# Performance work log

Measured on AMD Instinct MI355X. Metric: run time of the kernel, lower is better.

## Reference

```python
import jax, jax.numpy as jnp
import numpy as np

B, S, D, H, DK, F, L, FEAT, T = 32, 256, 512, 8, 64, 2048, 6, 9, 100


def _pos_emb(seq_len, d):
    # 'transformers from scratch' style sinusoidal embedding
    pos = jnp.arange(seq_len, dtype=jnp.float32)[:, None]
    dim = jnp.arange(d, dtype=jnp.float32)[None, :]
    phase = pos / jnp.power(1e4, dim / d)
    return jnp.where(jnp.arange(d)[None, :] % 2 == 0, jnp.sin(phase), jnp.cos(phase))


def _ln(x, g, b, eps=1e-5):
    m = jnp.mean(x, -1, keepdims=True)
    v = jnp.mean((x - m) ** 2, -1, keepdims=True)
    return (x - m) * jax.lax.rsqrt(v + eps) * g + b


def _mha(q_in, k_in, v_in, wq, bq, wk, bk, wv, bv, wo, bo):
    # wq/wk/wv: [H, D, DK]; batched equivalent of per-head Linear projections
    q = jnp.einsum('bsd,hdk->bhsk', q_in, wq) + bq[:, None, :]
    k = jnp.einsum('bsd,hdk->bhsk', k_in, wk) + bk[:, None, :]
    v = jnp.einsum('bsd,hdk->bhsk', v_in, wv) + bv[:, None, :]
    scale = jnp.sqrt(jnp.asarray(q.shape[-1], jnp.float32))
    att = jax.nn.softmax(jnp.einsum('bhqk,bhsk->bhqs', q, k) / scale, axis=-1)
    o = jnp.einsum('bhqs,bhsv->bhqv', att, v)  # [B,H,S,DK]
    o = o.transpose(0, 2, 1, 3).reshape(q_in.shape[0], q_in.shape[1], -1)  # concat heads
    return o @ wo + bo


def setup_inputs() -> dict:
    key = jax.random.key(0)
    ks = iter(jax.random.split(key, 64))
    rn = lambda *sh: 0.02 * jax.random.normal(next(ks), sh, jnp.float32)
    d = {
        'tgt': jax.random.uniform(next(ks), (B, S, FEAT), jnp.float32),
        'memory': jax.random.normal(next(ks), (B, S, D), jnp.float32),
        'time': jax.random.randint(next(ks), (B, S), 0, T),
        'gender': jax.random.randint(next(ks), (B, 1), 0, 2),
        'race': jax.random.randint(next(ks), (B, 1), 0, 3),
        'mask': jax.random.uniform(next(ks), (B, S, FEAT), jnp.float32),
        'w_f2h': rn(FEAT, D), 'b_f2h': jnp.zeros((D,)),
        'emb_time': rn(T, D), 'emb_gender': rn(2, D), 'emb_race': rn(3, D),
        'wq1': rn(L, H, D, DK), 'bq1': jnp.zeros((L, H, DK)),
        'wk1': rn(L, H, D, DK), 'bk1': jnp.zeros((L, H, DK)),
        'wv1': rn(L, H, D, DK), 'bv1': jnp.zeros((L, H, DK)),
        'wo1': rn(L, H * DK, D), 'bo1': jnp.zeros((L, D)),
        'g1': jnp.ones((L, D)), 'be1': jnp.zeros((L, D)),
        'wq2': rn(L, H, D, DK), 'bq2': jnp.zeros((L, H, DK)),
        'wk2': rn(L, H, D, DK), 'bk2': jnp.zeros((L, H, DK)),
        'wv2': rn(L, H, D, DK), 'bv2': jnp.zeros((L, H, DK)),
        'wo2': rn(L, H * DK, D), 'bo2': jnp.zeros((L, D)),
        'g2': jnp.ones((L, D)), 'be2': jnp.zeros((L, D)),
        'w1f': rn(L, D, F), 'b1f': jnp.zeros((L, F)),
        'w2f': rn(L, F, D), 'b2f': jnp.zeros((L, D)),
        'gf': jnp.ones((L, D)), 'bff': jnp.zeros((L, D)),
        'w_out': rn(D, FEAT), 'b_out': jnp.zeros((FEAT,)),
        'w_m': rn(D, FEAT), 'b_m': jnp.zeros((FEAT,)),
    }
    return d


def reference(tgt, memory, time, gender, race, mask,
              w_f2h, b_f2h, emb_time, emb_gender, emb_race,
              wq1, bq1, wk1, bk1, wv1, bv1, wo1, bo1, g1, be1,
              wq2, bq2, wk2, bk2, wv2, bv2, wo2, bo2, g2, be2,
              w1f, b1f, w2f, b2f, gf, bff,
              w_out, b_out, w_m, b_m):
    # attentioned_mask=False, mask provided -> tgt = tgt * mask
    x = (tgt * mask) @ w_f2h + b_f2h  # feature2hidden
    x = x + _pos_emb(x.shape[1], x.shape[2])
    x = x + emb_time[time] + emb_gender[gender] + emb_race[race]  # [B,S,D] += [B,1,D]
    for l in range(L):
        # self-attention residual block (dropout is identity in eval)
        x = _ln(x + _mha(x, x, x, wq1[l], bq1[l], wk1[l], bk1[l], wv1[l], bv1[l], wo1[l], bo1[l]), g1[l], be1[l])
        # 'cross' block: q,k from memory, v from tgt; residual on tgt (tensors[-1])
        x = _ln(x + _mha(memory, memory, x, wq2[l], bq2[l], wk2[l], bk2[l], wv2[l], bv2[l], wo2[l], bo2[l]), g2[l], be2[l])
        # feed forward
        x = _ln(x + jax.nn.relu(x @ w1f[l] + b1f[l]) @ w2f[l] + b2f[l], gf[l], bff[l])
    output = jax.nn.sigmoid(x @ w_out + b_out)
    mask_out = jax.nn.sigmoid(x @ w_m + b_m)  # attentioned_mask=False -> linear_m(tgt)
    return output, time, mask_out
```

## Files before the change

kernel.cpp:

```cpp
#include <hip/hip_runtime.h>
#include <hip/hip_bf16.h>
#include <math.h>

constexpr int Bn   = 32;
constexpr int Sn   = 256;
constexpr int Dn   = 512;
constexpr int Hn   = 8;
constexpr int DKn  = 64;
constexpr int Fn   = 2048;
constexpr int Ln   = 6;
constexpr int FEATn= 9;
constexpr int BSn  = Bn * Sn;

typedef __hip_bfloat16 bf16;
typedef __attribute__((ext_vector_type(8))) short short8;
typedef __attribute__((ext_vector_type(4))) short short4v;
typedef __attribute__((ext_vector_type(4))) float f32x4;

#define GLOAD_LDS16(gp, lp)                                                   \
    __builtin_amdgcn_global_load_lds(                                         \
        (const __attribute__((address_space(1))) void*)(gp),                  \
        (__attribute__((address_space(3))) void*)(lp), 16, 0, 0)

#define BARRIER do {                                                          \
    __builtin_amdgcn_sched_barrier(0);                                        \
    asm volatile("" ::: "memory");                                            \
    __builtin_amdgcn_s_barrier();                                             \
    asm volatile("" ::: "memory");                                            \
    __builtin_amdgcn_sched_barrier(0);                                        \
} while (0)

#define VMCNT0 do {                                                           \
    asm volatile("s_waitcnt vmcnt(0)" ::: "memory");                          \
    __builtin_amdgcn_sched_barrier(0);                                        \
} while (0)

#define LGKM0 do {                                                            \
    asm volatile("s_waitcnt lgkmcnt(0)" ::: "memory");                        \
    __builtin_amdgcn_sched_barrier(0);                                        \
} while (0)

__device__ __forceinline__ short f2bs(float f) {
    __hip_bfloat16 h = __float2bfloat16(f);
    return *reinterpret_cast<short*>(&h);
}
__device__ __forceinline__ float bs2f(short s) {
    unsigned u = ((unsigned)(unsigned short)s) << 16;
    return *reinterpret_cast<float*>(&u);
}

__global__ __launch_bounds__(256)
void k_embed(const float* __restrict__ tgt, const float* __restrict__ mask,
             const float* __restrict__ w_f2h, const float* __restrict__ b_f2h,
             const int* __restrict__ timei, const int* __restrict__ gender,
             const int* __restrict__ race,
             const float* __restrict__ emb_t, const float* __restrict__ emb_g,
             const float* __restrict__ emb_r, bf16* __restrict__ x)
{
    int idx = blockIdx.x * 256 + threadIdx.x;
    int d  = idx & (Dn - 1);
    int bs = idx >> 9;
    int b  = bs / Sn;
    int s  = bs & (Sn - 1);
    const float* tg = tgt  + (size_t)bs * FEATn;
    const float* mk = mask + (size_t)bs * FEATn;
    float acc = b_f2h[d];
    #pragma unroll
    for (int f = 0; f < FEATn; ++f) acc += tg[f] * mk[f] * w_f2h[f * Dn + d];
    float phase = (float)s * expf(-((float)d / (float)Dn) * 9.210340372f);
    acc += (d & 1) ? cosf(phase) : sinf(phase);
    acc += emb_t[(size_t)timei[bs] * Dn + d];
    acc += emb_g[(size_t)gender[b] * Dn + d];
    acc += emb_r[(size_t)race[b]   * Dn + d];
    x[idx] = __float2bfloat16(acc);
}

__global__ __launch_bounds__(256)
void k_cvt(const float* __restrict__ in, bf16* __restrict__ out)
{
    int i = blockIdx.x * 256 + threadIdx.x;
    out[i] = __float2bfloat16(in[i]);
}

__global__ __launch_bounds__(256)
void k_tcvt6(const float* __restrict__ i0, bf16* __restrict__ o0,
             const float* __restrict__ i1, bf16* __restrict__ o1,
             const float* __restrict__ i2, bf16* __restrict__ o2,
             const float* __restrict__ i3, bf16* __restrict__ o3,
             const float* __restrict__ i4, bf16* __restrict__ o4,
             const float* __restrict__ i5, bf16* __restrict__ o5,
             int R, int C, int ZB)
{
    __shared__ float ts[32][33];
    const int sel = blockIdx.z / ZB, zi = blockIdx.z % ZB;
    const float* in  = sel == 0 ? i0 : sel == 1 ? i1 : sel == 2 ? i2
                     : sel == 3 ? i3 : sel == 4 ? i4 : i5;
    bf16*        out = sel == 0 ? o0 : sel == 1 ? o1 : sel == 2 ? o2
                     : sel == 3 ? o3 : sel == 4 ? o4 : o5;
    const int t  = threadIdx.x;
    const int tx = t & 31, ty = t >> 5;
    const int r0 = blockIdx.y * 32, c0 = blockIdx.x * 32;
    const size_t zo = (size_t)zi * R * C;
    #pragma unroll
    for (int i = 0; i < 4; ++i)
        ts[ty + 8 * i][tx] = in[zo + (size_t)(r0 + ty + 8 * i) * C + c0 + tx];
    __syncthreads();
    #pragma unroll
    for (int i = 0; i < 4; ++i)
        out[zo + (size_t)(c0 + ty + 8 * i) * R + r0 + tx] =
            __float2bfloat16(ts[tx][ty + 8 * i]);
}

__global__ __launch_bounds__(256)
void k_prep_final(const float* __restrict__ w_out, const float* __restrict__ b_out,
                  const float* __restrict__ w_m, const float* __restrict__ b_m,
                  bf16* __restrict__ Wcat, float* __restrict__ bcat)
{
    int idx = blockIdx.x * 256 + threadIdx.x;
    int n = idx >> 9, k = idx & 511;
    float v = 0.f;
    if (n < FEATn)          v = w_out[(size_t)k * FEATn + n];
    else if (n < 2 * FEATn) v = w_m[(size_t)k * FEATn + (n - FEATn)];
    Wcat[idx] = __float2bfloat16(v);
    if (idx < 32) {
        float bv = idx < FEATn ? b_out[idx]
                 : (idx < 2 * FEATn ? b_m[idx - FEATn] : 0.f);
        bcat[idx] = bv;
    }
}

template<int BM, int BN, bool RELU, bool RESID, bool TRANSV = false>
__global__ __launch_bounds__(256)
void k_gemm_bf(const bf16* __restrict__ A0, const bf16* __restrict__ A1,
               const bf16* __restrict__ A2,
               const bf16* __restrict__ W0, const bf16* __restrict__ W1,
               const bf16* __restrict__ W2,
               const float* __restrict__ bi0, const float* __restrict__ bi1,
               const float* __restrict__ bi2,
               const bf16* __restrict__ R,
               bf16* __restrict__ C0, bf16* __restrict__ C1, bf16* __restrict__ C2,
               int M, int N, int K, int MTt, int NTt, int ZN, int stat)
{
    constexpr int WTM = BM / 2, WTN = BN / 2;
    constexpr int MT  = WTM / 16, NT = WTN / 16;
    constexpr int NCA = BM / 64;
    constexpr int NCB = BN / 64;
    constexpr int CSTR   = BN + 8;
    constexpr int PASSES = BM / 64;

    const int id = blockIdx.x;
    const int c  = id & 7, j = id >> 3;
    int mt, nt, z;
    if (stat == 0) {
        const int inner = NTt * ZN;
        const int ml = j / inner, r = j - ml * inner;
        mt = c * (MTt >> 3) + ml;
        nt = r % NTt;
        z  = r / NTt;
    } else {
        const int inner = MTt * ZN;
        const int nl = j / inner, r = j - nl * inner;
        nt = c * (NTt >> 3) + nl;
        mt = r % MTt;
        z  = r / MTt;
    }
    const int m0 = mt * BM, n0 = nt * BN;

    const short* A   = (const short*)(z == 0 ? A0 : (z == 1 ? A1 : A2));
    const short* W   = (const short*)(z == 0 ? W0 : (z == 1 ? W1 : W2));
    const float* bia = (z == 0 ? bi0 : (z == 1 ? bi1 : bi2));
    bf16*        C   = (z == 0 ? C0 : (z == 1 ? C1 : C2));

    __shared__ __align__(16) short As[BM * 32];
    __shared__ __align__(16) short Bs[BN * 32];
    __shared__ __align__(16) short Cs[64 * CSTR];

    const int t    = threadIdx.x;
    const int w    = t >> 6, lane = t & 63;
    const int l16  = lane & 15, quad = lane >> 4;
    const int wm   = (w & 1) * WTM, wn = (w >> 1) * WTN;

    const short* Agp[NCA];
    const short* Bgp[NCB];
    #pragma unroll
    for (int i = 0; i < NCA; ++i) {
        const int cc = w * BM + i * 64 + lane;
        Agp[i] = A + (size_t)(m0 + (cc >> 2)) * K + (cc & 3) * 8;
    }
    #pragma unroll
    for (int i = 0; i < NCB; ++i) {
        const int cc = w * BN + i * 64 + lane;
        Bgp[i] = W + (size_t)(n0 + (cc >> 2)) * K + (cc & 3) * 8;
    }

    f32x4 acc[MT][NT] = {};
    const bool tv = TRANSV && (z == 2);

    for (int k0 = 0; k0 < K; k0 += 32) {
        #pragma unroll
        for (int i = 0; i < NCA; ++i) {
            GLOAD_LDS16(Agp[i], As + (w * BM + i * 64) * 8);
            Agp[i] += 32;
        }
        #pragma unroll
        for (int i = 0; i < NCB; ++i) {
            GLOAD_LDS16(Bgp[i], Bs + (w * BN + i * 64) * 8);
            Bgp[i] += 32;
        }
        __syncthreads();

        short8 af[MT], bf[NT];
        #pragma unroll
        for (int mi = 0; mi < MT; ++mi)
            af[mi] = *(const short8*)(As + (wm + mi * 16 + l16) * 32 + quad * 8);
        #pragma unroll
        for (int ni = 0; ni < NT; ++ni)
            bf[ni] = *(const short8*)(Bs + (wn + ni * 16 + l16) * 32 + quad * 8);
        if (tv) {
            #pragma unroll
            for (int mi = 0; mi < MT; ++mi)
                #pragma unroll
                for (int ni = 0; ni < NT; ++ni)
                    acc[mi][ni] = __builtin_amdgcn_mfma_f32_16x16x32_bf16(
                        bf[ni], af[mi], acc[mi][ni], 0, 0, 0);
        } else {
            #pragma unroll
            for (int mi = 0; mi < MT; ++mi)
                #pragma unroll
                for (int ni = 0; ni < NT; ++ni)
                    acc[mi][ni] = __builtin_amdgcn_mfma_f32_16x16x32_bf16(
                        af[mi], bf[ni], acc[mi][ni], 0, 0, 0);
        }
        __syncthreads();
    }

    if (tv) {
        constexpr int CPR = BM / 8;
        #pragma unroll
        for (int p = 0; p < PASSES; ++p) {
            if (PASSES == 1 || wn == p * 64) {
                #pragma unroll
                for (int ni = 0; ni < NT; ++ni) {
                    #pragma unroll
                    for (int r = 0; r < 4; ++r) {
                        const int lrow = wn - p * 64 + ni * 16 + quad * 4 + r;
                        const float bb = bia[n0 + p * 64 + lrow];
                        #pragma unroll
                        for (int mi = 0; mi < MT; ++mi)
                            Cs[lrow * CSTR + wm + mi * 16 + l16] =
                                f2bs(acc[mi][ni][r] + bb);
                    }
                }
            }
            __syncthreads();
            #pragma unroll
            for (int cc = 0; cc < 64 * CPR; cc += 256) {
                const int row = (cc + t) / CPR, colc = (cc + t) % CPR;
                short8 cv = *(const short8*)(Cs + row * CSTR + colc * 8);
                *(short8*)((short*)C + (size_t)(n0 + p * 64 + row) * M
                                      + m0 + colc * 8) = cv;
            }
            __syncthreads();
        }
    } else {
        constexpr int CPR = BN / 8;
        #pragma unroll
        for (int p = 0; p < PASSES; ++p) {
            if (PASSES == 1 || wm == p * 64) {
                #pragma unroll
                for (int ni = 0; ni < NT; ++ni) {
                    const float bb = bia[n0 + wn + ni * 16 + l16];
                    #pragma unroll
                    for (int mi = 0; mi < MT; ++mi) {
                        const int lrow0 = wm - p * 64 + mi * 16 + quad * 4;
                        #pragma unroll
                        for (int r = 0; r < 4; ++r) {
                            float v = acc[mi][ni][r] + bb;
                            if (RELU) v = fmaxf(v, 0.f);
                            Cs[(lrow0 + r) * CSTR + wn + ni * 16 + l16] = f2bs(v);
                        }
                    }
                }
            }
            __syncthreads();
            #pragma unroll
            for (int cc = 0; cc < 64 * CPR; cc += 256) {
                const int row = (cc + t) / CPR, colc = (cc + t) % CPR;
                const size_t goff = (size_t)(m0 + p * 64 + row) * N + n0 + colc * 8;
                short8 cv = *(const short8*)(Cs + row * CSTR + colc * 8);
                if (RESID) {
                    short8 rv = *(const short8*)((const short*)R + goff);
                    short8 ov;
                    #pragma unroll
                    for (int i = 0; i < 8; ++i)
                        ov[i] = f2bs(bs2f(cv[i]) + bs2f(rv[i]));
                    *(short8*)((short*)C + goff) = ov;
                } else {
                    *(short8*)((short*)C + goff) = cv;
                }
            }
            __syncthreads();
        }
    }
}

template<int RH, int CH, class STG, class FIN>
__device__ __forceinline__ void gemm8_phase(short* sm, int buf, int baseA,
                                            int baseB, f32x4 (&acc)[8][4],
                                            STG stg, FIN fin)
{
    short8 paf[2][4];
    short8 pbf[2][2];
    #pragma unroll
    for (int i = 0; i < 4; ++i) {
        const int a0 = buf + baseA + RH * 4096 + i * 1024;
        paf[0][i] = *(const short8*)(sm + a0);
        paf[1][i] = *(const short8*)(sm + (a0 ^ 32));
    }
    #pragma unroll
    for (int j = 0; j < 2; ++j) {
        const int b0 = buf + baseB + CH * 2048 + j * 1024;
        pbf[0][j] = *(const short8*)(sm + b0);
        pbf[1][j] = *(const short8*)(sm + (b0 ^ 32));
    }
    stg();
    BARRIER;
    __builtin_amdgcn_s_setprio(1);
    #pragma unroll
    for (int i = 0; i < 4; ++i)
        #pragma unroll
        for (int j = 0; j < 2; ++j) {
            acc[RH * 4 + i][CH * 2 + j] = __builtin_amdgcn_mfma_f32_16x16x32_bf16(
                paf[0][i], pbf[0][j], acc[RH * 4 + i][CH * 2 + j], 0, 0, 0);
            acc[RH * 4 + i][CH * 2 + j] = __builtin_amdgcn_mfma_f32_16x16x32_bf16(
                paf[1][i], pbf[1][j], acc[RH * 4 + i][CH * 2 + j], 0, 0, 0);
        }
    __builtin_amdgcn_s_setprio(0);
    fin();
    BARRIER;
}

template<bool RELU>
__global__ __launch_bounds__(512, 2)
void k_gemm8ph(const bf16* __restrict__ Ain, const bf16* __restrict__ Win,
               const float* __restrict__ bia, bf16* __restrict__ Cout,
               int M, int N, int K, int NTt)
{
    __shared__ __align__(16) short smem[65536];

    const int id  = blockIdx.x;
    const int cxd = id & 7, jj = id >> 3;
    const int mpx = (M >> 8) >> 3;
    const int ml  = jj / NTt, nl = jj % NTt;
    const int mt  = cxd * mpx + ml;
    const int m0  = mt * 256, n0 = nl * 256;

    const int t    = threadIdx.x;
    const int lane = t & 63, w = t >> 6;
    const int l16  = lane & 15, quad = lane >> 4;
    const int wr   = w >> 2, wc = w & 3;

    const short* A = (const short*)Ain;
    const short* W = (const short*)Win;

    const int rowL = t >> 3;
    const int cX   = (t & 7) ^ (rowL & 7);
    const short* pA00 = A + (size_t)(m0 +   0 +  0 + rowL) * K + cX * 8;
    const short* pA01 = A + (size_t)(m0 +   0 + 64 + rowL) * K + cX * 8;
    const short* pA10 = A + (size_t)(m0 + 128 +  0 + rowL) * K + cX * 8;
    const short* pA11 = A + (size_t)(m0 + 128 + 64 + rowL) * K + cX * 8;
    const short* pB00 = W + (size_t)(n0 +   0 +  0 + rowL) * K + cX * 8;
    const short* pB01 = W + (size_t)(n0 +   0 + 64 + rowL) * K + cX * 8;
    const short* pB10 = W + (size_t)(n0 + 128 +  0 + rowL) * K + cX * 8;
    const short* pB11 = W + (size_t)(n0 + 128 + 64 + rowL) * K + cX * 8;

    auto stageA = [&](int nb, int k2) {
        short* d = smem + nb * 16384 + t * 8;
        GLOAD_LDS16(pA00 + (size_t)k2 * 64, d);
        GLOAD_LDS16(pA01 + (size_t)k2 * 64, d + 4096);
        GLOAD_LDS16(pA10 + (size_t)k2 * 64, d + 8192);
        GLOAD_LDS16(pA11 + (size_t)k2 * 64, d + 12288);
    };
    auto stageB = [&](int nb, int k2) {
        short* d = smem + 32768 + nb * 16384 + t * 8;
        GLOAD_LDS16(pB00 + (size_t)k2 * 64, d);
        GLOAD_LDS16(pB01 + (size_t)k2 * 64, d + 4096);
        GLOAD_LDS16(pB10 + (size_t)k2 * 64, d + 8192);
        GLOAD_LDS16(pB11 + (size_t)k2 * 64, d + 12288);
    };

    const int axor  = (quad ^ (l16 & 7)) << 3;
    const int baseA = wr * 8192 + l16 * 64 + axor;
    const int baseB = 32768 + (wc >> 1) * 8192 + (wc & 1) * 4096
                    + l16 * 64 + axor;

    float bias_v[4];
    #pragma unroll
    for (int ni = 0; ni < 4; ++ni)
        bias_v[ni] = bia[n0 + wc * 64 + ni * 16 + l16];

    f32x4 acc[8][4] = {};

    stageA(0, 0);
    stageB(0, 0);
    VMCNT0;
    BARRIER;

    const int NKT = K >> 6;
    for (int kt = 0; kt < NKT; ++kt) {
        const int  buf = (kt & 1) << 14;
        const int  nb  = (kt + 1) & 1;
        const bool st  = (kt + 1) < NKT;
        gemm8_phase<0, 0>(smem, buf, baseA, baseB, acc,
                          [&] { if (st) stageA(nb, kt + 1); }, [&] {});
        gemm8_phase<0, 1>(smem, buf, baseA, baseB, acc,
                          [&] { if (st) stageB(nb, kt + 1); }, [&] {});
        gemm8_phase<1, 0>(smem, buf, baseA, baseB, acc, [&] {}, [&] {});
        gemm8_phase<1, 1>(smem, buf, baseA, baseB, acc, [&] {}, [&] { VMCNT0; });
    }

    #pragma unroll
    for (int p = 0; p < 2; ++p) {
        if (wr == p) {
            #pragma unroll
            for (int mi = 0; mi < 8; ++mi)
                #pragma unroll
                for (int ni = 0; ni < 4; ++ni)
                    #pragma unroll
                    for (int r = 0; r < 4; ++r) {
                        float v = acc[mi][ni][r] + bias_v[ni];
                        if (RELU) v = fmaxf(v, 0.f);
                        smem[(mi * 16 + quad * 4 + r) * 264
                             + wc * 64 + ni * 16 + l16] = f2bs(v);
                    }
        }
        LGKM0;
        BARRIER;
        #pragma unroll
        for (int i2 = 0; i2 < 8; ++i2) {
            const int idx = i2 * 512 + t;
            const int row = idx >> 5, chn = idx & 31;
            short8 cv = *(const short8*)(smem + row * 264 + chn * 8);
            *(short8*)((short*)Cout + (size_t)(m0 + p * 128 + row) * N
                                     + n0 + chn * 8) = cv;
        }
        LGKM0;
        BARRIER;
    }
}

__global__ __launch_bounds__(512, 2)
void k_qkv8ph(const bf16* __restrict__ Aqk, const bf16* __restrict__ Av,
              const bf16* __restrict__ Wq, const bf16* __restrict__ Wk,
              const bf16* __restrict__ Wv,
              const float* __restrict__ bq, const float* __restrict__ bk,
              const float* __restrict__ bv,
              bf16* __restrict__ Cq, bf16* __restrict__ Ck,
              bf16* __restrict__ Vt)
{
    __shared__ __align__(16) short smem[65536];

    constexpr int K = Dn;
    const int id  = blockIdx.x;
    const int cxd = id & 7, jj = id >> 3;
    const int ml  = jj / 6, nl = jj % 6;
    const int mt  = cxd * 4 + ml;
    const int m0  = mt * 256;
    const int sel = nl >> 1;
    const int n0l = (nl & 1) * 256;

    const short* A = (const short*)(sel < 2 ? Aqk : Av);
    const short* W = (const short*)(sel == 0 ? Wq : sel == 1 ? Wk : Wv);
    const float* bia = sel == 0 ? bq : sel == 1 ? bk : bv;

    const int t    = threadIdx.x;
    const int lane = t & 63, w = t >> 6;
    const int l16  = lane & 15, quad = lane >> 4;
    const int wr   = w >> 2, wc = w & 3;

    const int rowL = t >> 3;
    const int cX   = (t & 7) ^ (rowL & 7);
    const short* pA00 = A + (size_t)(m0 +   0 +  0 + rowL) * K + cX * 8;
    const short* pA01 = A + (size_t)(m0 +   0 + 64 + rowL) * K + cX * 8;
    const short* pA10 = A + (size_t)(m0 + 128 +  0 + rowL) * K + cX * 8;
    const short* pA11 = A + (size_t)(m0 + 128 + 64 + rowL) * K + cX * 8;
    const short* pB00 = W + (size_t)(n0l +   0 +  0 + rowL) * K + cX * 8;
    const short* pB01 = W + (size_t)(n0l +   0 + 64 + rowL) * K + cX * 8;
    const short* pB10 = W + (size_t)(n0l + 128 +  0 + rowL) * K + cX * 8;
    const short* pB11 = W + (size_t)(n0l + 128 + 64 + rowL) * K + cX * 8;

    auto stageA = [&](int nb, int k2) {
        short* d = smem + nb * 16384 + t * 8;
        GLOAD_LDS16(pA00 + (size_t)k2 * 64, d);
        GLOAD_LDS16(pA01 + (size_t)k2 * 64, d + 4096);
        GLOAD_LDS16(pA10 + (size_t)k2 * 64, d + 8192);
        GLOAD_LDS16(pA11 + (size_t)k2 * 64, d + 12288);
    };
    auto stageB = [&](int nb, int k2) {
        short* d = smem + 32768 + nb * 16384 + t * 8;
        GLOAD_LDS16(pB00 + (size_t)k2 * 64, d);
        GLOAD_LDS16(pB01 + (size_t)k2 * 64, d + 4096);
        GLOAD_LDS16(pB10 + (size_t)k2 * 64, d + 8192);
        GLOAD_LDS16(pB11 + (size_t)k2 * 64, d + 12288);
    };

    const int axor  = (quad ^ (l16 & 7)) << 3;
    const int baseA = wr * 8192 + l16 * 64 + axor;
    const int baseB = 32768 + (wc >> 1) * 8192 + (wc & 1) * 4096
                    + l16 * 64 + axor;

    float bias_v[4];
    #pragma unroll
    for (int ni = 0; ni < 4; ++ni)
        bias_v[ni] = bia[n0l + wc * 64 + ni * 16 + l16];

    f32x4 acc[8][4] = {};

    stageA(0, 0);
    stageB(0, 0);
    VMCNT0;
    BARRIER;

    constexpr int NKT = K >> 6;
    for (int kt = 0; kt < NKT; ++kt) {
        const int  buf = (kt & 1) << 14;
        const int  nb  = (kt + 1) & 1;
        const bool st  = (kt + 1) < NKT;
        gemm8_phase<0, 0>(smem, buf, baseA, baseB, acc,
                          [&] { if (st) stageA(nb, kt + 1); }, [&] {});
        gemm8_phase<0, 1>(smem, buf, baseA, baseB, acc,
                          [&] { if (st) stageB(nb, kt + 1); }, [&] {});
        gemm8_phase<1, 0>(smem, buf, baseA, baseB, acc, [&] {}, [&] {});
        gemm8_phase<1, 1>(smem, buf, baseA, baseB, acc, [&] {}, [&] { VMCNT0; });
    }

    if (sel < 2) {
        bf16* C = sel == 0 ? Cq : Ck;
        #pragma unroll
        for (int p = 0; p < 2; ++p) {
            if (wr == p) {
                #pragma unroll
                for (int mi = 0; mi < 8; ++mi)
                    #pragma unroll
                    for (int ni = 0; ni < 4; ++ni)
                        #pragma unroll
                        for (int r = 0; r < 4; ++r)
                            smem[(mi * 16 + quad * 4 + r) * 264
                                 + wc * 64 + ni * 16 + l16] =
                                f2bs(acc[mi][ni][r] + bias_v[ni]);
            }
            LGKM0;
            BARRIER;
            #pragma unroll
            for (int i2 = 0; i2 < 8; ++i2) {
                const int idx = i2 * 512 + t;
                const int row = idx >> 5, chn = idx & 31;
                short8 cv = *(const short8*)(smem + row * 264 + chn * 8);
                *(short8*)((short*)C + (size_t)(m0 + p * 128 + row) * Dn
                                     + n0l + chn * 8) = cv;
            }
            LGKM0;
            BARRIER;
        }
    } else {
        #pragma unroll
        for (int p = 0; p < 4; ++p) {
            if (wc == p) {
                #pragma unroll
                for (int mi = 0; mi < 8; ++mi)
                    #pragma unroll
                    for (int ni = 0; ni < 4; ++ni)
                        #pragma unroll
                        for (int r = 0; r < 4; ++r)
                            smem[(ni * 16 + l16) * 264
                                 + wr * 128 + mi * 16 + quad * 4 + r] =
                                f2bs(acc[mi][ni][r] + bias_v[ni]);
            }
            LGKM0;
            BARRIER;
            #pragma unroll
            for (int i2 = 0; i2 < 4; ++i2) {
                const int idx = i2 * 512 + t;
                const int row = idx >> 5, chn = idx & 31;
                short8 cv = *(const short8*)(smem + row * 264 + chn * 8);
                *(short8*)((short*)Vt + (size_t)(n0l + p * 64 + row) * BSn
                                      + m0 + chn * 8) = cv;
            }
            LGKM0;
            BARRIER;
        }
    }
}

__global__ __launch_bounds__(256)
void k_attn_mfma(const bf16* __restrict__ q, const bf16* __restrict__ k,
                 const bf16* __restrict__ vT, bf16* __restrict__ ocat)
{
    __shared__ __align__(16) short smem[33280];
    short* Vst = smem;
    short* Ks  = smem + 16384;
    short* Ps  = smem + 16384;
    short* Cs  = smem + 16384;

    const int t = threadIdx.x, w = t >> 6, lane = t & 63;
    const int l16 = lane & 15, quad = lane >> 4;
    const int qt = blockIdx.x >> 8;
    const int bh = blockIdx.x & 255;
    const int h  = bh & 7;
    const int b  = bh >> 3;
    const int q0 = qt * 64;

    const short* kg = (const short*)k  + (size_t)b * Sn * Dn + h * DKn;
    const short* qg = (const short*)q  + (size_t)b * Sn * Dn + h * DKn;
    const short* vg = (const short*)vT + (size_t)h * DKn * BSn + b * Sn;

    #pragma unroll
    for (int i = 0; i < 8; ++i) {
        const int c   = w * 512 + i * 64 + lane;
        const int key = c >> 3, cgk = (c & 7) ^ (key & 7);
        GLOAD_LDS16(kg + (size_t)key * Dn + cgk * 8, Ks + (w * 512 + i * 64) * 8);
        const int dv = c >> 5, cgv = (c & 31) ^ (dv & 7);
        GLOAD_LDS16(vg + (size_t)dv * BSn + cgv * 8, Vst + (w * 512 + i * 64) * 8);
    }

    const short* qp = qg + (size_t)(q0 + w * 16 + l16) * Dn + quad * 8;
    short8 bq0 = *(const short8*)(qp);
    short8 bq1 = *(const short8*)(qp + 32);
    __syncthreads();

    f32x4 accs[16];
    #pragma unroll
    for (int mi = 0; mi < 16; ++mi) accs[mi] = f32x4{0.f, 0.f, 0.f, 0.f};
    #pragma unroll
    for (int mi = 0; mi < 16; ++mi) {
        const int key = mi * 16 + l16;
        const int r0s = (quad     ^ (key & 7)) * 8;
        const int r1s = ((quad+4) ^ (key & 7)) * 8;
        short8 af0 = *(const short8*)(Ks + key * 64 + r0s);
        short8 af1 = *(const short8*)(Ks + key * 64 + r1s);
        accs[mi] = __builtin_amdgcn_mfma_f32_16x16x32_bf16(af0, bq0, accs[mi], 0, 0, 0);
        accs[mi] = __builtin_amdgcn_mfma_f32_16x16x32_bf16(af1, bq1, accs[mi], 0, 0, 0);
    }

    float mx = -1e30f;
    #pragma unroll
    for (int mi = 0; mi < 16; ++mi)
        #pragma unroll
        for (int r = 0; r < 4; ++r) mx = fmaxf(mx, accs[mi][r]);
    mx = fmaxf(mx, __shfl_xor(mx, 16));
    mx = fmaxf(mx, __shfl_xor(mx, 32));
    float sum = 0.f;
    #pragma unroll
    for (int mi = 0; mi < 16; ++mi)
        #pragma unroll
        for (int r = 0; r < 4; ++r) {
            float e = __expf((accs[mi][r] - mx) * 0.125f);
            accs[mi][r] = e;
            sum += e;
        }
    sum += __shfl_xor(sum, 16);
    sum += __shfl_xor(sum, 32);
    const float rs = 1.f / sum;

    __syncthreads();

    short* pr = Ps + (w * 16 + l16) * 264;
    #pragma unroll
    for (int mi = 0; mi < 16; ++mi) {
        short4v pk;
        pk.x = f2bs(accs[mi][0] * rs);
        pk.y = f2bs(accs[mi][1] * rs);
        pk.z = f2bs(accs[mi][2] * rs);
        pk.w = f2bs(accs[mi][3] * rs);
        *(short4v*)(pr + mi * 16 + quad * 4) = pk;
    }
    __syncthreads();

    f32x4 acco[4];
    #pragma unroll
    for (int nt = 0; nt < 4; ++nt) acco[nt] = f32x4{0.f, 0.f, 0.f, 0.f};
    #pragma unroll
    for (int k0 = 0; k0 < 8; ++k0) {
        short8 pa = *(const short8*)(pr + k0 * 32 + quad * 8);
        #pragma unroll
        for (int nt = 0; nt < 4; ++nt) {
            const int dv = nt * 16 + l16;
            const int sl = ((4 * k0 + quad) ^ (dv & 7)) * 8;
            short8 vb = *(const short8*)(Vst + dv * 256 + sl);
            acco[nt] = __builtin_amdgcn_mfma_f32_16x16x32_bf16(pa, vb, acco[nt], 0, 0, 0);
        }
    }
    __syncthreads();

    #pragma unroll
    for (int nt = 0; nt < 4; ++nt)
        #pragma unroll
        for (int r = 0; r < 4; ++r)
            Cs[(w * 16 + quad * 4 + r) * 72 + nt * 16 + l16] = f2bs(acco[nt][r]);
    __syncthreads();
    #pragma unroll
    for (int c = 0; c < 512; c += 256) {
        const int row = (c + t) >> 3, colc = (c + t) & 7;
        short8 cv = *(const short8*)(Cs + row * 72 + colc * 8);
        *(short8*)((short*)ocat + (size_t)(b * Sn + q0 + row) * Dn
                                 + h * DKn + colc * 8) = cv;
    }
}

__global__ __launch_bounds__(256)
void k_ln(const bf16* __restrict__ y, const float* __restrict__ g,
          const float* __restrict__ be, bf16* __restrict__ xo)
{
    const int t = threadIdx.x, w = t >> 6, lane = t & 63;
    const int row = blockIdx.x * 4 + w;
    const short* yr = (const short*)y + (size_t)row * Dn + lane * 8;
    short8 v8 = *(const short8*)yr;
    float f[8];
    float s1 = 0.f, s2 = 0.f;
    #pragma unroll
    for (int i = 0; i < 8; ++i) {
        f[i] = bs2f(v8[i]);
        s1 += f[i];
        s2 += f[i] * f[i];
    }
    #pragma unroll
    for (int off = 1; off < 64; off <<= 1) {
        s1 += __shfl_xor(s1, off);
        s2 += __shfl_xor(s2, off);
    }
    const float mean = s1 * (1.f / Dn);
    const float var  = s2 * (1.f / Dn) - mean * mean;
    const float isd  = rsqrtf(var + 1e-5f);
    const float4 g0 = *(const float4*)(g  + lane * 8);
    const float4 g1 = *(const float4*)(g  + lane * 8 + 4);
    const float4 b0 = *(const float4*)(be + lane * 8);
    const float4 b1 = *(const float4*)(be + lane * 8 + 4);
    const float gg[8] = {g0.x, g0.y, g0.z, g0.w, g1.x, g1.y, g1.z, g1.w};
    const float bb[8] = {b0.x, b0.y, b0.z, b0.w, b1.x, b1.y, b1.z, b1.w};
    short8 o8;
    #pragma unroll
    for (int i = 0; i < 8; ++i)
        o8[i] = f2bs((f[i] - mean) * isd * gg[i] + bb[i]);
    *(short8*)((short*)xo + (size_t)row * Dn + lane * 8) = o8;
}

__global__ __launch_bounds__(256)
void k_final2(const bf16* __restrict__ x, const bf16* __restrict__ Wcat,
              const float* __restrict__ bcat, const int* __restrict__ timei,
              float* __restrict__ out)
{
    const int t = threadIdx.x, w = t >> 6, lane = t & 63;
    const int l16 = lane & 15, quad = lane >> 4;
    const int r0 = blockIdx.x * 64 + w * 16;
    const short* xp = (const short*)x + (size_t)(r0 + l16) * Dn + quad * 8;
    const short* wp = (const short*)Wcat + (size_t)l16 * Dn + quad * 8;

    f32x4 acc[2] = {};
    #pragma unroll
    for (int kk = 0; kk < 16; ++kk) {
        short8 af = *(const short8*)(xp + kk * 32);
        short8 b0 = *(const short8*)(wp + kk * 32);
        short8 b1 = *(const short8*)(wp + 16 * Dn + kk * 32);
        acc[0] = __builtin_amdgcn_mfma_f32_16x16x32_bf16(af, b0, acc[0], 0, 0, 0);
        acc[1] = __builtin_amdgcn_mfma_f32_16x16x32_bf16(af, b1, acc[1], 0, 0, 0);
    }

    #pragma unroll
    for (int nt = 0; nt < 2; ++nt) {
        const int col = nt * 16 + l16;
        const float bb = bcat[col];
        #pragma unroll
        for (int r = 0; r < 4; ++r) {
            const int row = r0 + quad * 4 + r;
            float v = acc[nt][r] + bb;
            float sg = 1.f / (1.f + expf(-v));
            if (col < FEATn)
                out[(size_t)row * FEATn + col] = sg;
            else if (col < 2 * FEATn)
                out[(size_t)BSn * FEATn + BSn + (size_t)row * FEATn + (col - FEATn)] = sg;
        }
    }
    if (l16 == 0) {
        #pragma unroll
        for (int r = 0; r < 4; ++r) {
            const int row = r0 + quad * 4 + r;
            out[(size_t)BSn * FEATn + row] = (float)timei[row];
        }
    }
}

extern "C" void kernel_launch(void* const* d_in, const int* in_sizes, int n_in,
                              void* d_out, int out_size, void* d_ws, size_t ws_size,
                              hipStream_t stream)
{
    const float* tgt    = (const float*)d_in[0];
    const float* memory = (const float*)d_in[1];
    const int*   timei  = (const int*)  d_in[2];
    const int*   gender = (const int*)  d_in[3];
    const int*   race   = (const int*)  d_in[4];
    const float* maskp  = (const float*)d_in[5];
    const float* w_f2h  = (const float*)d_in[6];
    const float* b_f2h  = (const float*)d_in[7];
    const float* emb_t  = (const float*)d_in[8];
    const float* emb_g  = (const float*)d_in[9];
    const float* emb_r  = (const float*)d_in[10];
    const float* wq1 = (const float*)d_in[11]; const float* bq1 = (const float*)d_in[12];
    const float* wk1 = (const float*)d_in[13]; const float* bk1 = (const float*)d_in[14];
    const float* wv1 = (const float*)d_in[15]; const float* bv1 = (const float*)d_in[16];
    const float* wo1 = (const float*)d_in[17]; const float* bo1 = (const float*)d_in[18];
    const float* g1  = (const float*)d_in[19]; const float* be1 = (const float*)d_in[20];
    const float* wq2 = (const float*)d_in[21]; const float* bq2 = (const float*)d_in[22];
    const float* wk2 = (const float*)d_in[23]; const float* bk2 = (const float*)d_in[24];
    const float* wv2 = (const float*)d_in[25]; const float* bv2 = (const float*)d_in[26];
    const float* wo2 = (const float*)d_in[27]; const float* bo2 = (const float*)d_in[28];
    const float* g2  = (const float*)d_in[29]; const float* be2 = (const float*)d_in[30];
    const float* w1f = (const float*)d_in[31]; const float* b1f = (const float*)d_in[32];
    const float* w2f = (const float*)d_in[33]; const float* b2f = (const float*)d_in[34];
    const float* gfp = (const float*)d_in[35]; const float* bff = (const float*)d_in[36];
    const float* w_out = (const float*)d_in[37]; const float* b_out = (const float*)d_in[38];
    const float* w_m   = (const float*)d_in[39]; const float* b_m   = (const float*)d_in[40];
    float* out = (float*)d_out;

    constexpr size_t WH  = 1572864;
    constexpr size_t WF  = 6291456;
    constexpr size_t NA  = (size_t)BSn * Dn;
    bf16* wsb   = (bf16*)d_ws;
    bf16* wq1t  = wsb;
    bf16* wk1t  = wq1t + WH;
    bf16* wv1t  = wk1t + WH;
    bf16* wo1t  = wv1t + WH;
    bf16* wq2t  = wo1t + WH;
    bf16* wk2t  = wq2t + WH;
    bf16* wv2t  = wk2t + WH;
    bf16* wo2t  = wv2t + WH;
    bf16* w1ft  = wo2t + WH;
    bf16* w2ft  = w1ft + WF;
    bf16* memb  = w2ft + WF;
    bf16* x     = memb + NA;
    bf16* b1    = x  + NA;
    bf16* b2    = b1 + NA;
    bf16* b3    = b2 + NA;
    bf16* b4    = b3 + NA;
    bf16* h1    = b1;
    bf16* wcat  = b4 + NA;
    float* bcat = (float*)(wcat + 32 * Dn);

    dim3 blk(256);

    k_tcvt6<<<dim3( 2, 16, 288), blk, 0, stream>>>(
        wq1, wq1t, wk1, wk1t, wv1, wv1t, wq2, wq2t, wk2, wk2t, wv2, wv2t,
        512, 64, 48);
    k_tcvt6<<<dim3(16, 16, 12), blk, 0, stream>>>(
        wo1, wo1t, wo2, wo2t, wo1, wo1t, wo1, wo1t, wo1, wo1t, wo1, wo1t,
        512, 512, 6);
    k_tcvt6<<<dim3(64, 16, 6), blk, 0, stream>>>(
        w1f, w1ft, w1f, w1ft, w1f, w1ft, w1f, w1ft, w1f, w1ft, w1f, w1ft,
        512, 2048, 6);
    k_tcvt6<<<dim3(16, 64, 6), blk, 0, stream>>>(
        w2f, w2ft, w2f, w2ft, w2f, w2ft, w2f, w2ft, w2f, w2ft, w2f, w2ft,
        2048, 512, 6);
    k_cvt <<<dim3(NA / 256), blk, 0, stream>>>(memory, memb);
    k_prep_final<<<dim3(64), blk, 0, stream>>>(w_out, b_out, w_m, b_m, wcat, bcat);

    k_embed<<<dim3((BSn * Dn) / 256), blk, 0, stream>>>(
        tgt, maskp, w_f2h, b_f2h, timei, gender, race, emb_t, emb_g, emb_r, x);

    dim3 gQ (192);
    dim3 gP6(128 * 8);
    dim3 g8 (32 * 8);
    dim3 blk8(512);
    dim3 gA (Bn * Hn * 4);
    dim3 gL (BSn / 4);
    constexpr size_t WSL = 262144;
    constexpr size_t WFL = 1048576;

    for (int l = 0; l < Ln; ++l) {
        k_qkv8ph<<<gQ, blk8, 0, stream>>>(
            x, x,
            wq1t + l * WSL, wk1t + l * WSL, wv1t + l * WSL,
            bq1 + l * Dn, bk1 + l * Dn, bv1 + l * Dn,
            b1, b2, b3);
        k_attn_mfma<<<gA, blk, 0, stream>>>(b1, b2, b3, b4);
        k_gemm_bf<64, 64, false, true><<<gP6, blk, 0, stream>>>(
            b4, b4, b4, wo1t + l * WSL, wo1t + l * WSL, wo1t + l * WSL,
            bo1 + l * Dn, bo1 + l * Dn, bo1 + l * Dn,
            x, x, x, x, BSn, Dn, Dn, 128, 8, 1, 0);
        k_ln<<<gL, blk, 0, stream>>>(x, g1 + l * Dn, be1 + l * Dn, x);
        k_qkv8ph<<<gQ, blk8, 0, stream>>>(
            memb, x,
            wq2t + l * WSL, wk2t + l * WSL, wv2t + l * WSL,
            bq2 + l * Dn, bk2 + l * Dn, bv2 + l * Dn,
            b1, b2, b3);
        k_attn_mfma<<<gA, blk, 0, stream>>>(b1, b2, b3, b4);
        k_gemm_bf<64, 64, false, true><<<gP6, blk, 0, stream>>>(
            b4, b4, b4, wo2t + l * WSL, wo2t + l * WSL, wo2t + l * WSL,
            bo2 + l * Dn, bo2 + l * Dn, bo2 + l * Dn,
            x, x, x, x, BSn, Dn, Dn, 128, 8, 1, 0);
        k_ln<<<gL, blk, 0, stream>>>(x, g2 + l * Dn, be2 + l * Dn, x);
        k_gemm8ph<true><<<g8, blk8, 0, stream>>>(
            x, w1ft + l * WFL, b1f + l * Fn, h1, BSn, Fn, Dn, 8);
        k_gemm_bf<64, 64, false, true><<<gP6, blk, 0, stream>>>(
            h1, h1, h1, w2ft + l * WFL, w2ft + l * WFL, w2ft + l * WFL,
            b2f + l * Dn, b2f + l * Dn, b2f + l * Dn,
            x, x, x, x, BSn, Dn, Fn, 128, 8, 1, 0);
        k_ln<<<gL, blk, 0, stream>>>(x, gfp + l * Dn, bff + l * Dn, x);
    }

    k_final2<<<dim3(BSn / 64), blk, 0, stream>>>(x, wcat, bcat, timei, out);
}
```

Before: 1.381 ms.

## Replace generic 64x64 GEMM with double-buffered swizzled-LDS kernel for output and FFN2 projections

Replaces the generic k_gemm_bf (used for the attention output projections and the second FFN GEMM) with a specialized 64x64-tile kernel. The new kernel uses K-steps of 64 and double-buffers the LDS tiles, issuing the next stage's async global-to-LDS loads before the current MFMAs so memory and compute overlap. It also XOR-swizzles the LDS layout to cut bank conflicts, raises wave priority around the MFMA block, and preloads the bias values. The trade-off is 32KB of shared memory per block, which may reduce occupancy, and the kernel drops the multi-Z and transposed-output generality.

```diff
diff --git a/kernel.cpp b/kernel.cpp
--- a/kernel.cpp
+++ b/kernel.cpp
@@ -129,177 +129,118 @@
     }
 }
 
-template<int BM, int BN, bool RELU, bool RESID, bool TRANSV = false>
+template<bool RELU, bool RESID>
 __global__ __launch_bounds__(256)
-void k_gemm_bf(const bf16* __restrict__ A0, const bf16* __restrict__ A1,
-               const bf16* __restrict__ A2,
-               const bf16* __restrict__ W0, const bf16* __restrict__ W1,
-               const bf16* __restrict__ W2,
-               const float* __restrict__ bi0, const float* __restrict__ bi1,
-               const float* __restrict__ bi2,
-               const bf16* __restrict__ R,
-               bf16* __restrict__ C0, bf16* __restrict__ C1, bf16* __restrict__ C2,
-               int M, int N, int K, int MTt, int NTt, int ZN, int stat)
-{
-    constexpr int WTM = BM / 2, WTN = BN / 2;
-    constexpr int MT  = WTM / 16, NT = WTN / 16;
-    constexpr int NCA = BM / 64;
-    constexpr int NCB = BN / 64;
-    constexpr int CSTR   = BN + 8;
-    constexpr int PASSES = BM / 64;
+void k_gemm2ph(const bf16* __restrict__ Ain, const bf16* __restrict__ Win,
+               const float* __restrict__ bia, const bf16* __restrict__ Rr,
+               bf16* __restrict__ Cout, int M, int N, int K, int MTt, int NTt)
+{
+    __shared__ __align__(16) short smem[16384];
 
     const int id = blockIdx.x;
-    const int c  = id & 7, j = id >> 3;
-    int mt, nt, z;
-    if (stat == 0) {
-        const int inner = NTt * ZN;
-        const int ml = j / inner, r = j - ml * inner;
-        mt = c * (MTt >> 3) + ml;
-        nt = r % NTt;
-        z  = r / NTt;
-    } else {
-        const int inner = MTt * ZN;
-        const int nl = j / inner, r = j - nl * inner;
-        nt = c * (NTt >> 3) + nl;
-        mt = r % MTt;
-        z  = r / MTt;
-    }
-    const int m0 = mt * BM, n0 = nt * BN;
-
-    const short* A   = (const short*)(z == 0 ? A0 : (z == 1 ? A1 : A2));
-    const short* W   = (const short*)(z == 0 ? W0 : (z == 1 ? W1 : W2));
-    const float* bia = (z == 0 ? bi0 : (z == 1 ? bi1 : bi2));
-    bf16*        C   = (z == 0 ? C0 : (z == 1 ? C1 : C2));
-
-    __shared__ __align__(16) short As[BM * 32];
-    __shared__ __align__(16) short Bs[BN * 32];
-    __shared__ __align__(16) short Cs[64 * CSTR];
-
-    const int t    = threadIdx.x;
-    const int w    = t >> 6, lane = t & 63;
-    const int l16  = lane & 15, quad = lane >> 4;
-    const int wm   = (w & 1) * WTM, wn = (w >> 1) * WTN;
-
-    const short* Agp[NCA];
-    const short* Bgp[NCB];
-    #pragma unroll
-    for (int i = 0; i < NCA; ++i) {
-        const int cc = w * BM + i * 64 + lane;
-        Agp[i] = A + (size_t)(m0 + (cc >> 2)) * K + (cc & 3) * 8;
-    }
-    #pragma unroll
-    for (int i = 0; i < NCB; ++i) {
-        const int cc = w * BN + i * 64 + lane;
-        Bgp[i] = W + (size_t)(n0 + (cc >> 2)) * K + (cc & 3) * 8;
-    }
-
-    f32x4 acc[MT][NT] = {};
-    const bool tv = TRANSV && (z == 2);
-
-    for (int k0 = 0; k0 < K; k0 += 32) {
-        #pragma unroll
-        for (int i = 0; i < NCA; ++i) {
-            GLOAD_LDS16(Agp[i], As + (w * BM + i * 64) * 8);
-            Agp[i] += 32;
-        }
-        #pragma unroll
-        for (int i = 0; i < NCB; ++i) {
-            GLOAD_LDS16(Bgp[i], Bs + (w * BN + i * 64) * 8);
-            Bgp[i] += 32;
-        }
-        __syncthreads();
-
-        short8 af[MT], bf[NT];
-        #pragma unroll
-        for (int mi = 0; mi < MT; ++mi)
-            af[mi] = *(const short8*)(As + (wm + mi * 16 + l16) * 32 + quad * 8);
-        #pragma unroll
-        for (int ni = 0; ni < NT; ++ni)
-            bf[ni] = *(const short8*)(Bs + (wn + ni * 16 + l16) * 32 + quad * 8);
-        if (tv) {
+    const int cx = id & 7, j = id >> 3;
+    const int mt = cx * (MTt >> 3) + j / NTt;
+    const int nt = j % NTt;
+    const int m0 = mt * 64, n0 = nt * 64;
+
+    const int t = threadIdx.x, w = t >> 6, lane = t & 63;
+    const int l16 = lane & 15, quad = lane >> 4;
+    const int wm = (w & 1) * 32, wn = (w >> 1) * 32;
+
+    const short* A = (const short*)Ain;
+    const short* W = (const short*)Win;
+
+    const int rowL = t >> 3;
+    const int cX   = (t & 7) ^ (rowL & 7);
+    const short* pA0 = A + (size_t)(m0 +  0 + rowL) * K + cX * 8;
+    const short* pA1 = A + (size_t)(m0 + 32 + rowL) * K + cX * 8;
+    const short* pB0 = W + (size_t)(n0 +  0 + rowL) * K + cX * 8;
+    const short* pB1 = W + (size_t)(n0 + 32 + rowL) * K + cX * 8;
+
+    auto stage = [&](int nb, int k2) {
+        short* dA = smem + nb * 4096 + t * 8;
+        short* dB = smem + 8192 + nb * 4096 + t * 8;
+        GLOAD_LDS16(pA0 + (size_t)k2 * 64, dA);
+        GLOAD_LDS16(pA1 + (size_t)k2 * 64, dA + 2048);
+        GLOAD_LDS16(pB0 + (size_t)k2 * 64, dB);
+        GLOAD_LDS16(pB1 + (size_t)k2 * 64, dB + 2048);
+    };
+
+    const int axor  = (quad ^ (l16 & 7)) << 3;
+    const int aBase = (wm + l16) * 64 + axor;
+    const int bBase = 8192 + (wn + l16) * 64 + axor;
+
+    float bias_v[2];
+    #pragma unroll
+    for (int ni = 0; ni < 2; ++ni)
+        bias_v[ni] = bia[n0 + wn + ni * 16 + l16];
+
+    f32x4 acc[2][2] = {};
+
+    stage(0, 0);
+    VMCNT0;
+    BARRIER;
+
+    const int NKT = K >> 6;
+    for (int kt = 0; kt < NKT; ++kt) {
+        const int buf = (kt & 1) * 4096;
+        short8 af[2][2], bw[2][2];
+        #pragma unroll
+        for (int mi = 0; mi < 2; ++mi) {
+            const int a0 = buf + aBase + mi * 1024;
+            af[0][mi] = *(const short8*)(smem + a0);
+            af[1][mi] = *(const short8*)(smem + (a0 ^ 32));
+        }
+        #pragma unroll
+        for (int ni = 0; ni < 2; ++ni) {
+            const int b0 = buf + bBase + ni * 1024;
+            bw[0][ni] = *(const short8*)(smem + b0);
+            bw[1][ni] = *(const short8*)(smem + (b0 ^ 32));
+        }
+        if (kt + 1 < NKT) stage((kt + 1) & 1, kt + 1);
+        LGKM0;
+        __builtin_amdgcn_s_setprio(1);
+        #pragma unroll
+        for (int ks = 0; ks < 2; ++ks)
             #pragma unroll
-            for (int mi = 0; mi < MT; ++mi)
+            for (int mi = 0; mi < 2; ++mi)
                 #pragma unroll
-                for (int ni = 0; ni < NT; ++ni)
+                for (int ni = 0; ni < 2; ++ni)
                     acc[mi][ni] = __builtin_amdgcn_mfma_f32_16x16x32_bf16(
-                        bf[ni], af[mi], acc[mi][ni], 0, 0, 0);
+                        af[ks][mi], bw[ks][ni], acc[mi][ni], 0, 0, 0);
+        __builtin_amdgcn_s_setprio(0);
+        VMCNT0;
+        BARRIER;
+    }
+
+    #pragma unroll
+    for (int mi = 0; mi < 2; ++mi)
+        #pragma unroll
+        for (int ni = 0; ni < 2; ++ni)
+            #pragma unroll
+            for (int r = 0; r < 4; ++r) {
+                float v = acc[mi][ni][r] + bias_v[ni];
+                if (RELU) v = fmaxf(v, 0.f);
+                smem[(wm + mi * 16 + quad * 4 + r) * 72
+                     + wn + ni * 16 + l16] = f2bs(v);
+            }
+    LGKM0;
+    BARRIER;
+    #pragma unroll
+    for (int i2 = 0; i2 < 2; ++i2) {
+        const int idx = i2 * 256 + t;
+        const int row = idx >> 3, colc = idx & 7;
+        const size_t goff = (size_t)(m0 + row) * N + n0 + colc * 8;
+        short8 cv = *(const short8*)(smem + row * 72 + colc * 8);
+        if (RESID) {
+            short8 rv = *(const short8*)((const short*)Rr + goff);
+            short8 ov;
+            #pragma unroll
+            for (int i = 0; i < 8; ++i)
+                ov[i] = f2bs(bs2f(cv[i]) + bs2f(rv[i]));
+            *(short8*)((short*)Cout + goff) = ov;
         } else {
-            #pragma unroll
-            for (int mi = 0; mi < MT; ++mi)
-                #pragma unroll
-                for (int ni = 0; ni < NT; ++ni)
-                    acc[mi][ni] = __builtin_amdgcn_mfma_f32_16x16x32_bf16(
-                        af[mi], bf[ni], acc[mi][ni], 0, 0, 0);
-        }
-        __syncthreads();
-    }
-
-    if (tv) {
-        constexpr int CPR = BM / 8;
-        #pragma unroll
-        for (int p = 0; p < PASSES; ++p) {
-            if (PASSES == 1 || wn == p * 64) {
-                #pragma unroll
-                for (int ni = 0; ni < NT; ++ni) {
-                    #pragma unroll
-                    for (int r = 0; r < 4; ++r) {
-                        const int lrow = wn - p * 64 + ni * 16 + quad * 4 + r;
-                        const float bb = bia[n0 + p * 64 + lrow];
-                        #pragma unroll
-                        for (int mi = 0; mi < MT; ++mi)
-                            Cs[lrow * CSTR + wm + mi * 16 + l16] =
-                                f2bs(acc[mi][ni][r] + bb);
-                    }
-                }
-            }
-            __syncthreads();
-            #pragma unroll
-            for (int cc = 0; cc < 64 * CPR; cc += 256) {
-                const int row = (cc + t) / CPR, colc = (cc + t) % CPR;
-                short8 cv = *(const short8*)(Cs + row * CSTR + colc * 8);
-                *(short8*)((short*)C + (size_t)(n0 + p * 64 + row) * M
-                                      + m0 + colc * 8) = cv;
-            }
-            __syncthreads();
-        }
-    } else {
-        constexpr int CPR = BN / 8;
-        #pragma unroll
-        for (int p = 0; p < PASSES; ++p) {
-            if (PASSES == 1 || wm == p * 64) {
-                #pragma unroll
-                for (int ni = 0; ni < NT; ++ni) {
-                    const float bb = bia[n0 + wn + ni * 16 + l16];
-                    #pragma unroll
-                    for (int mi = 0; mi < MT; ++mi) {
-                        const int lrow0 = wm - p * 64 + mi * 16 + quad * 4;
-                        #pragma unroll
-                        for (int r = 0; r < 4; ++r) {
-                            float v = acc[mi][ni][r] + bb;
-                            if (RELU) v = fmaxf(v, 0.f);
-                            Cs[(lrow0 + r) * CSTR + wn + ni * 16 + l16] = f2bs(v);
-                        }
-                    }
-                }
-            }
-            __syncthreads();
-            #pragma unroll
-            for (int cc = 0; cc < 64 * CPR; cc += 256) {
-                const int row = (cc + t) / CPR, colc = (cc + t) % CPR;
-                const size_t goff = (size_t)(m0 + p * 64 + row) * N + n0 + colc * 8;
-                short8 cv = *(const short8*)(Cs + row * CSTR + colc * 8);
-                if (RESID) {
-                    short8 rv = *(const short8*)((const short*)R + goff);
-                    short8 ov;
-                    #pragma unroll
-                    for (int i = 0; i < 8; ++i)
-                        ov[i] = f2bs(bs2f(cv[i]) + bs2f(rv[i]));
-                    *(short8*)((short*)C + goff) = ov;
-                } else {
-                    *(short8*)((short*)C + goff) = cv;
-                }
-            }
-            __syncthreads();
+            *(short8*)((short*)Cout + goff) = cv;
         }
     }
 }
@@ -866,7 +807,7 @@
         tgt, maskp, w_f2h, b_f2h, timei, gender, race, emb_t, emb_g, emb_r, x);
 
     dim3 gQ (192);
-    dim3 gP6(128 * 8);
+    dim3 gW (128 * 8);
     dim3 g8 (32 * 8);
     dim3 blk8(512);
     dim3 gA (Bn * Hn * 4);
@@ -881,10 +822,8 @@
             bq1 + l * Dn, bk1 + l * Dn, bv1 + l * Dn,
             b1, b2, b3);
         k_attn_mfma<<<gA, blk, 0, stream>>>(b1, b2, b3, b4);
-        k_gemm_bf<64, 64, false, true><<<gP6, blk, 0, stream>>>(
-            b4, b4, b4, wo1t + l * WSL, wo1t + l * WSL, wo1t + l * WSL,
-            bo1 + l * Dn, bo1 + l * Dn, bo1 + l * Dn,
-            x, x, x, x, BSn, Dn, Dn, 128, 8, 1, 0);
+        k_gemm2ph<false, true><<<gW, blk, 0, stream>>>(
+            b4, wo1t + l * WSL, bo1 + l * Dn, x, x, BSn, Dn, Dn, 128, 8);
         k_ln<<<gL, blk, 0, stream>>>(x, g1 + l * Dn, be1 + l * Dn, x);
         k_qkv8ph<<<gQ, blk8, 0, stream>>>(
             memb, x,
@@ -892,17 +831,13 @@
             bq2 + l * Dn, bk2 + l * Dn, bv2 + l * Dn,
             b1, b2, b3);
         k_attn_mfma<<<gA, blk, 0, stream>>>(b1, b2, b3, b4);
-        k_gemm_bf<64, 64, false, true><<<gP6, blk, 0, stream>>>(
-            b4, b4, b4, wo2t + l * WSL, wo2t + l * WSL, wo2t + l * WSL,
-            bo2 + l * Dn, bo2 + l * Dn, bo2 + l * Dn,
-            x, x, x, x, BSn, Dn, Dn, 128, 8, 1, 0);
+        k_gemm2ph<false, true><<<gW, blk, 0, stream>>>(
+            b4, wo2t + l * WSL, bo2 + l * Dn, x, x, BSn, Dn, Dn, 128, 8);
         k_ln<<<gL, blk, 0, stream>>>(x, g2 + l * Dn, be2 + l * Dn, x);
         k_gemm8ph<true><<<g8, blk8, 0, stream>>>(
             x, w1ft + l * WFL, b1f + l * Fn, h1, BSn, Fn, Dn, 8);
-        k_gemm_bf<64, 64, false, true><<<gP6, blk, 0, stream>>>(
-            h1, h1, h1, w2ft + l * WFL, w2ft + l * WFL, w2ft + l * WFL,
-            b2f + l * Dn, b2f + l * Dn, b2f + l * Dn,
-            x, x, x, x, BSn, Dn, Fn, 128, 8, 1, 0);
+        k_gemm2ph<false, true><<<gW, blk, 0, stream>>>(
+            h1, w2ft + l * WFL, b2f + l * Dn, x, x, BSn, Dn, Fn, 128, 8);
         k_ln<<<gL, blk, 0, stream>>>(x, gfp + l * Dn, bff + l * Dn, x);
     }
 
```

After: 1.313 ms. -4.9%, faster.
